# Kernel tuning notes

Measured on AMD Instinct MI355X. Metric: run time of the kernel, lower is better.

## Reference

```python
import jax, jax.numpy as jnp
import numpy as np

EPS = 1e-8
K_KNN = 20

def vn_lin(W, x):
    # W: [Cout, Cin], x: [B, Cin, 3, ...] -> [B, Cout, 3, ...]
    return jnp.einsum('oi,bi...->bo...', W, x)

def vn_relu(Wd, x):
    # VNLeakyReLU with negative_slope=0, share_nonlinearity=False
    d = jnp.einsum('oi,bi...->bo...', Wd, x)
    dot = jnp.sum(x * d, axis=2, keepdims=True)   # sum over 3-vector axis
    dsq = jnp.sum(d * d, axis=2, keepdims=True) + EPS
    return jnp.where(dot >= 0, x, x - (dot / dsq) * d)

def graph_feature_cross(p, k):
    # p: [B, N, 3] -> feat: [B, 3, 3, N, k]
    xx = jnp.sum(p * p, axis=-1)                       # [B,N]
    inner = jnp.einsum('bnd,bmd->bnm', p, p)           # [B,N,N]
    neg_dist = 2.0 * inner - xx[:, :, None] - xx[:, None, :]
    idx = jax.lax.top_k(neg_dist, k)[1]                # [B,N,k] nearest neighbors
    nbrs = jax.vmap(lambda pb, ib: pb[ib])(p, idx)     # [B,N,k,3]
    xr = jnp.broadcast_to(p[:, :, None, :], nbrs.shape)
    cross = jnp.cross(nbrs, xr)                        # [B,N,k,3]
    feat = jnp.stack([nbrs - xr, xr, cross], axis=3)   # [B,N,k,3(ch),3(vec)]
    return jnp.transpose(feat, (0, 3, 4, 1, 2))        # [B,3,3,N,k]

def setup_inputs() -> dict:
    key = jax.random.key(0)
    ks = jax.random.split(key, 9)
    B, N = 4, 2048
    H = 128           # hidden_dim // 3
    C_IN = 2 * H      # 256
    CC = 128          # c_dim // 3
    s_in = 1.0 / np.sqrt(C_IN)
    s_h = 1.0 / np.sqrt(H)
    return {
        'p': jax.random.normal(ks[0], (B, N, 3), dtype=jnp.float32),
        'fc_pos_W': jax.random.normal(ks[1], (C_IN, 3), dtype=jnp.float32) / np.sqrt(3.0),
        'blk_d0': jax.random.normal(ks[2], (5, C_IN, C_IN), dtype=jnp.float32) * s_in,
        'blk_W0': jax.random.normal(ks[3], (5, H, C_IN), dtype=jnp.float32) * s_in,
        'blk_d1': jax.random.normal(ks[4], (5, H, H), dtype=jnp.float32) * s_h,
        'blk_W1': jax.random.normal(ks[5], (5, H, H), dtype=jnp.float32) * s_h,
        'blk_Ws': jax.random.normal(ks[6], (5, H, C_IN), dtype=jnp.float32) * s_in,
        'fc_c_W': jax.random.normal(ks[7], (CC, H), dtype=jnp.float32) * s_h,
        'act_d': jax.random.normal(ks[8], (H, H), dtype=jnp.float32) * s_h,
    }

def reference(p, fc_pos_W, blk_d0, blk_W0, blk_d1, blk_W1, blk_Ws, fc_c_W, act_d):
    feat = graph_feature_cross(p, K_KNN)          # [B,3,3,N,k]
    x = vn_lin(fc_pos_W, feat)                    # [B,256,3,N,k]
    net = jnp.mean(x, axis=-1)                    # mean_pool over k -> [B,256,3,N]

    def block(i, x):
        h = vn_lin(blk_W0[i], vn_relu(blk_d0[i], x))
        dx = vn_lin(blk_W1[i], vn_relu(blk_d1[i], h))
        return vn_lin(blk_Ws[i], x) + dx          # shortcut (size_in != size_out)

    net = block(0, net)                           # [B,128,3,N]
    for i in range(1, 5):
        pooled = jnp.broadcast_to(jnp.mean(net, axis=3, keepdims=True), net.shape)
        net = block(i, jnp.concatenate([net, pooled], axis=1))
    net = jnp.mean(net, axis=3)                   # [B,128,3]
    c = vn_lin(fc_c_W, vn_relu(act_d, net))       # [B,128,3]
    return c.reshape(c.shape[0], -1)              # [B,384]
```

## Files before the change

kernel.cpp:

```cpp
#include <hip/hip_runtime.h>
#include <math.h>

#define N_PTS 2048
#define K_NN  20
#define K_D   10
#define WTOT  819200
#define NM_REP 8
#define NM_STRIDE 1536
#define NM_BLK (NM_REP*NM_STRIDE)
#define NBLK 256
#define BPB  64
#define ROWS 96
#define LDS_BYTES (2*ROWS*264*2)

typedef unsigned short u16;
typedef unsigned int   u32;
typedef _Float16 f16;
using half8   = __attribute__((ext_vector_type(8))) _Float16;
using floatx4 = __attribute__((ext_vector_type(4))) float;

__device__ __forceinline__ void split2h(float v, f16& h, f16& l) {
    h = (f16)v;
    l = (f16)((v - (float)h) * 1024.0f);
}

__device__ __forceinline__ float neg_dist(float4 q2, float4 c) {
    return fmaf(q2.x, c.x, fmaf(q2.y, c.y, fmaf(q2.z, c.z, -q2.w))) - c.w;
}

__global__ __launch_bounds__(256) void prep_kernel(
    const float* __restrict__ pts, float* __restrict__ m_out,
    const float* __restrict__ bd0, const float* __restrict__ bW0,
    const float* __restrict__ bd1, const float* __restrict__ bW1,
    const float* __restrict__ bWs, u16* __restrict__ Wswz,
    float* __restrict__ nm_acc)
{
    __shared__ float4 sp[N_PTS];
    if (blockIdx.x >= 1024) {
        int i = (blockIdx.x - 1024) * 256 + threadIdx.x;
        if (i >= WTOT) return;
        if (i < 5*NM_BLK + 32) nm_acc[i] = 0.f;
        float v; int base, K, local;
        if (i < 327680)      { int rel = i;          base = (rel/65536)*65536;            local = rel%65536; K = 256; v = bd0[rel]; }
        else if (i < 491520) { int rel = i - 327680; base = 327680 + (rel/32768)*32768;   local = rel%32768; K = 256; v = bW0[rel]; }
        else if (i < 573440) { int rel = i - 491520; base = 491520 + (rel/16384)*16384;   local = rel%16384; K = 128; v = bd1[rel]; }
        else if (i < 655360) { int rel = i - 573440; base = 573440 + (rel/16384)*16384;   local = rel%16384; K = 128; v = bW1[rel]; }
        else                 { int rel = i - 655360; base = 655360 + (rel/32768)*32768;   local = rel%32768; K = 256; v = bWs[rel]; }
        int m = local / K, k = local % K;
        int NKF = K >> 5;
        int mf = m >> 4, r = m & 15;
        int kf = k >> 5, q = (k >> 3) & 3, ii = k & 7;
        int lane = q*16 + r;
        int dst = base + ((mf*NKF + kf)*64 + lane)*8 + ii;
        f16 h, l; split2h(v, h, l);
        f16* W = (f16*)Wswz;
        W[dst] = h; W[WTOT + dst] = l;
        return;
    }

    const int b     = blockIdx.x >> 8;
    const int qbase = (blockIdx.x & 255) << 3;
    const int ql    = threadIdx.x >> 5;
    const int sl    = threadIdx.x & 31;
    const float* pb = pts + (size_t)b * N_PTS * 3;
    for (int i = threadIdx.x; i < N_PTS; i += 256) {
        float x = pb[i*3+0], y = pb[i*3+1], z = pb[i*3+2];
        sp[i] = make_float4(x, y, z, x*x + y*y + z*z);
    }
    __syncthreads();

    const int n = qbase + ql;
    const float4 q = sp[n];
    const float4 q2 = make_float4(2.f*q.x, 2.f*q.y, 2.f*q.z, q.w);

    float t[K_D];
#pragma unroll
    for (int s = 0; s < K_D; ++s) t[s] = -INFINITY;

    for (int j = 0; j < N_PTS/32; ++j) {
        float4 c = sp[j*32 + sl];
        float v = neg_dist(q2, c);
#pragma unroll
        for (int s = 0; s < K_D; ++s) {
            float nx = (s < K_D-1) ? t[s+1] : INFINITY;
            t[s] = fminf(fmaxf(t[s], v), nx);
        }
    }

    float head = t[K_D-1];
    float T = -INFINITY;
#pragma unroll 1
    for (int e = 0; e < K_NN; ++e) {
        float v = head; int w = sl;
#pragma unroll
        for (int off = 1; off < 32; off <<= 1) {
            float vo = __shfl_xor(v, off);
            int   wo = __shfl_xor(w, off);
            bool take = (vo > v) || (vo == v && wo < w);
            v = take ? vo : v;
            w = take ? wo : w;
        }
        T = v;
        if (w == sl) {
#pragma unroll
            for (int s = K_D-1; s > 0; --s) t[s] = t[s-1];
            t[0] = -INFINITY;
            head = t[K_D-1];
        }
    }

    float sx = 0.f, sy = 0.f, sz = 0.f;
    for (int j = 0; j < N_PTS/32; ++j) {
        float4 c = sp[j*32 + sl];
        float v = neg_dist(q2, c);
        if (v >= T) { sx += c.x; sy += c.y; sz += c.z; }
    }
#pragma unroll
    for (int off = 1; off < 32; off <<= 1) {
        sx += __shfl_xor(sx, off);
        sy += __shfl_xor(sy, off);
        sz += __shfl_xor(sz, off);
    }
    if (sl == 0) {
        const float inv = 1.0f / (float)K_NN;
        const int pt = b * N_PTS + n;
        m_out[pt*3+0] = sx * inv;
        m_out[pt*3+1] = sy * inv;
        m_out[pt*3+2] = sz * inv;
    }
}

template<int MF, int JF>
__device__ __forceinline__ void run_gemm_hi(
    const f16* __restrict__ Whi, size_t aoff,
    int NK, const f16* Blds, int bstride, int lane,
    floatx4 (&acc)[MF][JF])
{
    const int l15 = lane & 15;
    const int lq8 = (lane >> 4) * 8;
    half8 Aa[MF], Ab[MF];

    auto loada = [&](half8 (&dst)[MF], int kf) {
#pragma unroll
        for (int fm = 0; fm < MF; ++fm)
            dst[fm] = *(const half8*)(Whi + aoff + (size_t)(fm*NK + kf)*512 + (size_t)lane*8);
    };
    auto step = [&](half8 (&af)[MF], int kf) {
        half8 bq[JF];
#pragma unroll
        for (int fj = 0; fj < JF; ++fj)
            bq[fj] = *(const half8*)&Blds[(fj*16 + l15)*bstride + kf*32 + lq8];
#pragma unroll
        for (int fm = 0; fm < MF; ++fm)
#pragma unroll
            for (int fj = 0; fj < JF; ++fj)
                acc[fm][fj] = __builtin_amdgcn_mfma_f32_16x16x32_f16(af[fm], bq[fj], acc[fm][fj], 0, 0, 0);
    };

    loada(Aa, 0);
#pragma unroll 1
    for (int kf = 0; kf < NK; kf += 2) {
        loada(Ab, kf + 1);
        step(Aa, kf);
        if (kf + 2 < NK) loada(Aa, kf + 2);
        step(Ab, kf + 1);
    }
}

template<int MF, int JF>
__device__ __forceinline__ void run_gemm_split(
    const f16* __restrict__ Whi, const f16* __restrict__ Wlo, size_t aoff,
    int NK, const f16* Blds, int bstride, int lane,
    floatx4 (&acc)[MF][JF], floatx4 (&accL)[MF][JF])
{
    const int l15 = lane & 15;
    const int lq8 = (lane >> 4) * 8;
    half8 Aa[2*MF], Ab[2*MF];

    auto loada = [&](half8 (&dst)[2*MF], int kf) {
#pragma unroll
        for (int fm = 0; fm < MF; ++fm) {
            size_t fo = aoff + (size_t)(fm*NK + kf)*512 + (size_t)lane*8;
            dst[fm*2+0] = *(const half8*)(Whi + fo);
            dst[fm*2+1] = *(const half8*)(Wlo + fo);
        }
    };
    auto step = [&](half8 (&af)[2*MF], int kf) {
        half8 bq[JF];
#pragma unroll
        for (int fj = 0; fj < JF; ++fj)
            bq[fj] = *(const half8*)&Blds[(fj*16 + l15)*bstride + kf*32 + lq8];
#pragma unroll
        for (int fm = 0; fm < MF; ++fm)
#pragma unroll
            for (int fj = 0; fj < JF; ++fj) {
                acc[fm][fj]  = __builtin_amdgcn_mfma_f32_16x16x32_f16(af[fm*2+0], bq[fj], acc[fm][fj], 0, 0, 0);
                accL[fm][fj] = __builtin_amdgcn_mfma_f32_16x16x32_f16(af[fm*2+1], bq[fj], accL[fm][fj], 0, 0, 0);
            }
    };

    loada(Aa, 0);
#pragma unroll 1
    for (int kf = 0; kf < NK; kf += 2) {
        loada(Ab, kf + 1);
        step(Aa, kf);
        if (kf + 2 < NK) loada(Aa, kf + 2);
        step(Ab, kf + 1);
    }
}

__device__ __forceinline__ uint2 pack_res(floatx4 a, floatx4 aL) {
    u16 hh[4];
#pragma unroll
    for (int r = 0; r < 4; ++r) {
        f16 hv = (f16)(a[r] + aL[r] * (1.0f/1024.0f));
        hh[r] = *(u16*)&hv;
    }
    uint2 pv;
    pv.x = (u32)hh[0] | ((u32)hh[1] << 16);
    pv.y = (u32)hh[2] | ((u32)hh[3] << 16);
    return pv;
}

__device__ __forceinline__ uint2 pack_hi(floatx4 a) {
    u16 hh[4];
#pragma unroll
    for (int r = 0; r < 4; ++r) {
        f16 hv = (f16)a[r];
        hh[r] = *(u16*)&hv;
    }
    uint2 pv;
    pv.x = (u32)hh[0] | ((u32)hh[1] << 16);
    pv.y = (u32)hh[2] | ((u32)hh[3] << 16);
    return pv;
}

__global__ __launch_bounds__(512, 2) void resnet_kernel(
    const u16* __restrict__ Wswz,
    const float* __restrict__ pts, const float* __restrict__ m_buf,
    const float* __restrict__ fcW,
    float* __restrict__ nm_acc, int* __restrict__ cnt,
    const float* __restrict__ act_d, const float* __restrict__ fc_c,
    float* __restrict__ out)
{
    extern __shared__ char smem_raw[];
    f16*   X  = (f16*)smem_raw;
    f16*   Yd = X + ROWS*264;
    float* YC = (float*)Yd;

    const int tid   = threadIdx.x;
    const int bB    = blockIdx.x / BPB;
    const int lane  = tid & 63;
    const int wv    = tid >> 6;
    const int mwave = wv >> 1;
    const int ncol  = wv & 1;
    const f16* Whi = (const f16*)Wswz;
    const f16* Wlo = Whi + WTOT;

#pragma unroll 1
    for (int st = 0; st < 5; ++st) {
        const int offD0 = st*65536;
        const int offW0 = 327680 + st*32768;
        const int offD1 = 491520 + st*16384;
        const int offW1 = 573440 + st*16384;
        const int offWs = 655360 + st*32768;

        if (st == 0) {
            float* Hf = YC;
            const int ptbase = blockIdx.x * 32;
            for (int i = tid; i < 768; i += 512) Hf[i] = fcW[i];
            if (tid < 192) Hf[768 + tid] = (tid < 96) ? pts[ptbase*3 + tid]
                                                      : m_buf[ptbase*3 + tid - 96];
            __syncthreads();
#pragma unroll 1
            for (int it = 0; it < 6; ++it) {
                int idx = tid + 512*it;
                int r = idx >> 5;
                int cg = idx & 31;
                int l = r / 3, v = r - l*3;
                float pv0[3] = {Hf[768+l*3], Hf[768+l*3+1], Hf[768+l*3+2]};
                float mv0[3] = {Hf[864+l*3], Hf[864+l*3+1], Hf[864+l*3+2]};
                int v1 = (v==2) ? 0 : v+1;
                int v2 = (v==0) ? 2 : v-1;
                float av = mv0[v] - pv0[v];
                float bv = pv0[v];
                float cv = mv0[v1]*pv0[v2] - mv0[v2]*pv0[v1];
                half8 o;
#pragma unroll
                for (int k = 0; k < 8; ++k) {
                    int ch = cg*8 + k;
                    o[k] = (f16)(Hf[ch*3+0]*av + Hf[ch*3+1]*bv + Hf[ch*3+2]*cv);
                }
                *(half8*)&X[r*264 + cg*8] = o;
            }
            __syncthreads();
        }

        floatx4 acc4[2][3], accL4[2][3];
#pragma unroll
        for (int a = 0; a < 2; ++a)
#pragma unroll
            for (int b = 0; b < 3; ++b) { acc4[a][b] = (floatx4){0,0,0,0}; accL4[a][b] = (floatx4){0,0,0,0}; }

        {
            floatx4 acc[4][3];
#pragma unroll
            for (int a = 0; a < 4; ++a)
#pragma unroll
                for (int b = 0; b < 3; ++b) acc[a][b] = (floatx4){0,0,0,0};
            run_gemm_hi<4,3>(Whi, (size_t)offD0 + (size_t)mwave*16384, 8,
                             X + ncol*48*264, 264, lane, acc);
#pragma unroll
            for (int fm = 0; fm < 4; ++fm)
#pragma unroll
                for (int fj = 0; fj < 3; ++fj) {
                    int mloc = mwave*64 + fm*16 + (lane>>4)*4;
                    int jl   = ncol*48 + fj*16 + (lane & 15);
                    *(uint2*)&Yd[jl*264 + mloc] = pack_hi(acc[fm][fj]);
                }
        }
        __syncthreads();

        run_gemm_split<2,3>(Whi, Wlo, (size_t)offWs + (size_t)mwave*8192, 8,
                            X + ncol*48*264, 264, lane, acc4, accL4);

#pragma unroll 1
        for (int it = 0; it < 2; ++it) {
            int idx = tid + 512*it;
            int l = idx >> 5, cg = idx & 31;
            half8 xa = *(const half8*)&X[(l*3+0)*264 + cg*8];
            half8 xb = *(const half8*)&X[(l*3+1)*264 + cg*8];
            half8 xc = *(const half8*)&X[(l*3+2)*264 + cg*8];
            half8 da = *(const half8*)&Yd[(l*3+0)*264 + cg*8];
            half8 db = *(const half8*)&Yd[(l*3+1)*264 + cg*8];
            half8 dc = *(const half8*)&Yd[(l*3+2)*264 + cg*8];
            half8 ya, yb, yc;
#pragma unroll
            for (int k = 0; k < 8; ++k) {
                float x0 = (float)xa[k], x1 = (float)xb[k], x2 = (float)xc[k];
                float d0 = (float)da[k], d1 = (float)db[k], d2 = (float)dc[k];
                float dot = x0*d0 + x1*d1 + x2*d2;
                float y0, y1, y2;
                if (dot >= 0.f) { y0 = x0; y1 = x1; y2 = x2; }
                else {
                    float dsq = d0*d0 + d1*d1 + d2*d2 + 1e-8f;
                    float sc = dot / dsq;
                    y0 = x0 - sc*d0; y1 = x1 - sc*d1; y2 = x2 - sc*d2;
                }
                ya[k] = (f16)y0; yb[k] = (f16)y1; yc[k] = (f16)y2;
            }
            *(half8*)&Yd[(l*3+0)*264 + cg*8] = ya;
            *(half8*)&Yd[(l*3+1)*264 + cg*8] = yb;
            *(half8*)&Yd[(l*3+2)*264 + cg*8] = yc;
        }
        __syncthreads();

        {
            floatx4 acc[2][3], accL[2][3];
#pragma unroll
            for (int a = 0; a < 2; ++a)
#pragma unroll
                for (int b = 0; b < 3; ++b) { acc[a][b] = (floatx4){0,0,0,0}; accL[a][b] = (floatx4){0,0,0,0}; }
            run_gemm_split<2,3>(Whi, Wlo, (size_t)offW0 + (size_t)mwave*8192, 8,
                                Yd + ncol*48*264, 264, lane, acc, accL);
#pragma unroll
            for (int fm = 0; fm < 2; ++fm)
#pragma unroll
                for (int fj = 0; fj < 3; ++fj) {
                    int mloc = mwave*32 + fm*16 + (lane>>4)*4;
                    int jl   = ncol*48 + fj*16 + (lane & 15);
                    *(uint2*)&X[jl*136 + mloc] = pack_res(acc[fm][fj], accL[fm][fj]);
                }
        }
        __syncthreads();

        {
            floatx4 acc[2][3];
#pragma unroll
            for (int a = 0; a < 2; ++a)
#pragma unroll
                for (int b = 0; b < 3; ++b) acc[a][b] = (floatx4){0,0,0,0};
            run_gemm_hi<2,3>(Whi, (size_t)offD1 + (size_t)mwave*4096, 4,
                             X + ncol*48*136, 136, lane, acc);
#pragma unroll
            for (int fm = 0; fm < 2; ++fm)
#pragma unroll
                for (int fj = 0; fj < 3; ++fj) {
                    int mloc = mwave*32 + fm*16 + (lane>>4)*4;
                    int jl   = ncol*48 + fj*16 + (lane & 15);
                    *(uint2*)&Yd[jl*136 + mloc] = pack_hi(acc[fm][fj]);
                }
        }
        __syncthreads();

        {
            int l = tid >> 4, cg = tid & 15;
            half8 xa = *(const half8*)&X[(l*3+0)*136 + cg*8];
            half8 xb = *(const half8*)&X[(l*3+1)*136 + cg*8];
            half8 xc = *(const half8*)&X[(l*3+2)*136 + cg*8];
            half8 da = *(const half8*)&Yd[(l*3+0)*136 + cg*8];
            half8 db = *(const half8*)&Yd[(l*3+1)*136 + cg*8];
            half8 dc = *(const half8*)&Yd[(l*3+2)*136 + cg*8];
            half8 ya, yb, yc;
#pragma unroll
            for (int k = 0; k < 8; ++k) {
                float x0 = (float)xa[k], x1 = (float)xb[k], x2 = (float)xc[k];
                float d0 = (float)da[k], d1 = (float)db[k], d2 = (float)dc[k];
                float dot = x0*d0 + x1*d1 + x2*d2;
                float y0, y1, y2;
                if (dot >= 0.f) { y0 = x0; y1 = x1; y2 = x2; }
                else {
                    float dsq = d0*d0 + d1*d1 + d2*d2 + 1e-8f;
                    float sc = dot / dsq;
                    y0 = x0 - sc*d0; y1 = x1 - sc*d1; y2 = x2 - sc*d2;
                }
                ya[k] = (f16)y0; yb[k] = (f16)y1; yc[k] = (f16)y2;
            }
            *(half8*)&X[(l*3+0)*136 + cg*8] = ya;
            *(half8*)&X[(l*3+1)*136 + cg*8] = yb;
            *(half8*)&X[(l*3+2)*136 + cg*8] = yc;
        }
        __syncthreads();

        run_gemm_split<2,3>(Whi, Wlo, (size_t)offW1 + (size_t)mwave*4096, 4,
                            X + ncol*48*136, 136, lane, acc4, accL4);
        __syncthreads();

#pragma unroll
        for (int fm = 0; fm < 2; ++fm)
#pragma unroll
            for (int fj = 0; fj < 3; ++fj) {
                int mloc = mwave*32 + fm*16 + (lane>>4)*4;
                int jl   = ncol*48 + fj*16 + (lane & 15);
                floatx4 res;
#pragma unroll
                for (int r = 0; r < 4; ++r) res[r] = acc4[fm][fj][r] + accL4[fm][fj][r] * (1.0f/1024.0f);
                *(uint2*)&X[jl*264 + mloc] = pack_res(acc4[fm][fj], accL4[fm][fj]);
                *(floatx4*)&YC[jl*132 + mloc] = res;
            }
        __syncthreads();

        const int rsel = (blockIdx.x & (NM_REP-1)) * NM_STRIDE;
        float* nmS = nm_acc + (size_t)st*NM_BLK;
        if (tid < 384) {
            int v = tid >> 7, ch = tid & 127;
            float sum = 0.f;
#pragma unroll 1
            for (int pt = 0; pt < 32; ++pt) sum += YC[(pt*3+v)*132 + ch];
            atomicAdd(nmS + rsel + (bB*3+v)*128 + ch, sum);
        }
        asm volatile("s_waitcnt vmcnt(0)" ::: "memory");
        __syncthreads();
        if (tid == 0)
            __hip_atomic_fetch_add(&cnt[st*4+bB], 1, __ATOMIC_RELAXED, __HIP_MEMORY_SCOPE_AGENT);
        if (st == 4) break;

        if (tid == 0) {
            while (__hip_atomic_load(&cnt[st*4+bB], __ATOMIC_RELAXED, __HIP_MEMORY_SCOPE_AGENT) < BPB)
                __builtin_amdgcn_s_sleep(8);
        }
        __syncthreads();

        f16* nmT = Yd;
        if (tid < 384) {
            int v = tid >> 7, ch = tid & 127;
            float sum = 0.f;
#pragma unroll
            for (int rep = 0; rep < NM_REP; ++rep)
                sum += __hip_atomic_load(nmS + rep*NM_STRIDE + (bB*3+v)*128 + ch,
                                         __ATOMIC_RELAXED, __HIP_MEMORY_SCOPE_AGENT);
            nmT[tid] = (f16)(sum * (1.0f/2048.0f));
        }
        __syncthreads();
#pragma unroll 1
        for (int idx = tid; idx < 1536; idx += 512) {
            int r = idx >> 4;
            int cg = (idx & 15) + 16;
            int v = r % 3;
            *(half8*)&X[r*264 + cg*8] = *(const half8*)&nmT[v*128 + (cg-16)*8];
        }
        __syncthreads();
    }

    if (blockIdx.x < 4) {
        const int b = blockIdx.x;
        if (tid == 0) {
            while (__hip_atomic_load(&cnt[16+b], __ATOMIC_RELAXED, __HIP_MEMORY_SCOPE_AGENT) < BPB)
                __builtin_amdgcn_s_sleep(8);
        }
        __syncthreads();
        float* xs = (float*)smem_raw;
        float* ys = xs + 384;
        const float* nm4 = nm_acc + (size_t)4*NM_BLK;
        if (tid < 128) {
            int c = tid;
            float s0 = 0.f, s1 = 0.f, s2 = 0.f;
#pragma unroll
            for (int rep = 0; rep < NM_REP; ++rep) {
                s0 += __hip_atomic_load(nm4 + rep*NM_STRIDE + (b*3+0)*128 + c, __ATOMIC_RELAXED, __HIP_MEMORY_SCOPE_AGENT);
                s1 += __hip_atomic_load(nm4 + rep*NM_STRIDE + (b*3+1)*128 + c, __ATOMIC_RELAXED, __HIP_MEMORY_SCOPE_AGENT);
                s2 += __hip_atomic_load(nm4 + rep*NM_STRIDE + (b*3+2)*128 + c, __ATOMIC_RELAXED, __HIP_MEMORY_SCOPE_AGENT);
            }
            xs[c*3+0] = s0 * (1.0f/2048.0f);
            xs[c*3+1] = s1 * (1.0f/2048.0f);
            xs[c*3+2] = s2 * (1.0f/2048.0f);
        }
        __syncthreads();
        if (tid < 128) {
            int c = tid;
            float d0 = 0.f, d1 = 0.f, d2 = 0.f;
            for (int i = 0; i < 128; ++i) {
                float w = act_d[c*128 + i];
                d0 = fmaf(w, xs[i*3+0], d0);
                d1 = fmaf(w, xs[i*3+1], d1);
                d2 = fmaf(w, xs[i*3+2], d2);
            }
            float x0 = xs[c*3+0], x1 = xs[c*3+1], x2 = xs[c*3+2];
            float dot = x0*d0 + x1*d1 + x2*d2;
            float y0, y1, y2;
            if (dot >= 0.f) { y0 = x0; y1 = x1; y2 = x2; }
            else {
                float dsq = d0*d0 + d1*d1 + d2*d2 + 1e-8f;
                float sc = dot / dsq;
                y0 = x0 - sc*d0; y1 = x1 - sc*d1; y2 = x2 - sc*d2;
            }
            ys[c*3+0] = y0; ys[c*3+1] = y1; ys[c*3+2] = y2;
        }
        __syncthreads();
        if (tid < 128) {
            int c = tid;
            float o0 = 0.f, o1 = 0.f, o2 = 0.f;
            for (int i = 0; i < 128; ++i) {
                float w = fc_c[c*128 + i];
                o0 = fmaf(w, ys[i*3+0], o0);
                o1 = fmaf(w, ys[i*3+1], o1);
                o2 = fmaf(w, ys[i*3+2], o2);
            }
            out[b*384 + c*3 + 0] = o0;
            out[b*384 + c*3 + 1] = o1;
            out[b*384 + c*3 + 2] = o2;
        }
    }
}

extern "C" void kernel_launch(void* const* d_in, const int* in_sizes, int n_in,
                              void* d_out, int out_size, void* d_ws, size_t ws_size,
                              hipStream_t stream)
{
    const float* p      = (const float*)d_in[0];
    const float* fc_pos = (const float*)d_in[1];
    const float* bd0    = (const float*)d_in[2];
    const float* bW0    = (const float*)d_in[3];
    const float* bd1    = (const float*)d_in[4];
    const float* bW1    = (const float*)d_in[5];
    const float* bWs    = (const float*)d_in[6];
    const float* fc_c   = (const float*)d_in[7];
    const float* act_d  = (const float*)d_in[8];
    float* out = (float*)d_out;

    char* w = (char*)d_ws;
    float* m_buf  = (float*)w;  w += 98304;
    float* nm_acc = (float*)w;  w += (size_t)5*NM_BLK*4;
    int*   cnt    = (int*)w;    w += 128;
    u16*   Wswz   = (u16*)w;    w += (size_t)2*WTOT*2;

    static bool attr_set = false;
    if (!attr_set) {
        hipFuncSetAttribute((const void*)resnet_kernel,
                            hipFuncAttributeMaxDynamicSharedMemorySize, LDS_BYTES);
        attr_set = true;
    }

    prep_kernel<<<dim3(1024 + 3200), dim3(256), 0, stream>>>(
        p, m_buf, bd0, bW0, bd1, bW1, bWs, Wswz, nm_acc);

    resnet_kernel<<<dim3(NBLK), dim3(512), LDS_BYTES, stream>>>(
        Wswz, p, m_buf, fc_pos, nm_acc, cnt, act_d, fc_c, out);

    (void)in_sizes; (void)n_in; (void)out_size; (void)ws_size;
}
```

Before: 224.4 us.

## Overlap per-point half of block GEMMs with cross-block pooled-mean barrier wait

The first two GEMMs of each residual block (d0 and Ws) are split along K into the per-point-feature half and the pooled-mean half. The first half is computed before spinning on the cross-block counter for the previous stage's mean. The barrier wait, mean gather and broadcast into LDS now happen afterwards, followed by the remaining K half. This hides grid-wide synchronisation latency behind MFMA work, at the cost of keeping more accumulators live across the wait, which may raise register pressure.

```diff
diff --git a/kernel.cpp b/kernel.cpp
--- a/kernel.cpp
+++ b/kernel.cpp
@@ -133,7 +133,7 @@
 template<int MF, int JF>
 __device__ __forceinline__ void run_gemm_hi(
     const f16* __restrict__ Whi, size_t aoff,
-    int NK, const f16* Blds, int bstride, int lane,
+    int NK, int kf0, int kf1, const f16* Blds, int bstride, int lane,
     floatx4 (&acc)[MF][JF])
 {
     const int l15 = lane & 15;
@@ -157,12 +157,12 @@
                 acc[fm][fj] = __builtin_amdgcn_mfma_f32_16x16x32_f16(af[fm], bq[fj], acc[fm][fj], 0, 0, 0);
     };
 
-    loada(Aa, 0);
-#pragma unroll 1
-    for (int kf = 0; kf < NK; kf += 2) {
+    loada(Aa, kf0);
+#pragma unroll 1
+    for (int kf = kf0; kf < kf1; kf += 2) {
         loada(Ab, kf + 1);
         step(Aa, kf);
-        if (kf + 2 < NK) loada(Aa, kf + 2);
+        if (kf + 2 < kf1) loada(Aa, kf + 2);
         step(Ab, kf + 1);
     }
 }
@@ -170,7 +170,7 @@
 template<int MF, int JF>
 __device__ __forceinline__ void run_gemm_split(
     const f16* __restrict__ Whi, const f16* __restrict__ Wlo, size_t aoff,
-    int NK, const f16* Blds, int bstride, int lane,
+    int NK, int kf0, int kf1, const f16* Blds, int bstride, int lane,
     floatx4 (&acc)[MF][JF], floatx4 (&accL)[MF][JF])
 {
     const int l15 = lane & 15;
@@ -199,12 +199,12 @@
             }
     };
 
-    loada(Aa, 0);
-#pragma unroll 1
-    for (int kf = 0; kf < NK; kf += 2) {
+    loada(Aa, kf0);
+#pragma unroll 1
+    for (int kf = kf0; kf < kf1; kf += 2) {
         loada(Ab, kf + 1);
         step(Aa, kf);
-        if (kf + 2 < NK) loada(Aa, kf + 2);
+        if (kf + 2 < kf1) loada(Aa, kf + 2);
         step(Ab, kf + 1);
     }
 }
@@ -296,33 +296,78 @@
             __syncthreads();
         }
 
+        floatx4 acc1[4][3];
         floatx4 acc4[2][3], accL4[2][3];
 #pragma unroll
+        for (int a = 0; a < 4; ++a)
+#pragma unroll
+            for (int b = 0; b < 3; ++b) acc1[a][b] = (floatx4){0,0,0,0};
+#pragma unroll
         for (int a = 0; a < 2; ++a)
 #pragma unroll
             for (int b = 0; b < 3; ++b) { acc4[a][b] = (floatx4){0,0,0,0}; accL4[a][b] = (floatx4){0,0,0,0}; }
 
-        {
-            floatx4 acc[4][3];
-#pragma unroll
-            for (int a = 0; a < 4; ++a)
-#pragma unroll
-                for (int b = 0; b < 3; ++b) acc[a][b] = (floatx4){0,0,0,0};
-            run_gemm_hi<4,3>(Whi, (size_t)offD0 + (size_t)mwave*16384, 8,
-                             X + ncol*48*264, 264, lane, acc);
+        if (st == 0) {
+            run_gemm_hi<4,3>(Whi, (size_t)offD0 + (size_t)mwave*16384, 8, 0, 8,
+                             X + ncol*48*264, 264, lane, acc1);
 #pragma unroll
             for (int fm = 0; fm < 4; ++fm)
 #pragma unroll
                 for (int fj = 0; fj < 3; ++fj) {
                     int mloc = mwave*64 + fm*16 + (lane>>4)*4;
                     int jl   = ncol*48 + fj*16 + (lane & 15);
-                    *(uint2*)&Yd[jl*264 + mloc] = pack_hi(acc[fm][fj]);
-                }
-        }
-        __syncthreads();
-
-        run_gemm_split<2,3>(Whi, Wlo, (size_t)offWs + (size_t)mwave*8192, 8,
-                            X + ncol*48*264, 264, lane, acc4, accL4);
+                    *(uint2*)&Yd[jl*264 + mloc] = pack_hi(acc1[fm][fj]);
+                }
+            __syncthreads();
+            run_gemm_split<2,3>(Whi, Wlo, (size_t)offWs + (size_t)mwave*8192, 8, 0, 8,
+                                X + ncol*48*264, 264, lane, acc4, accL4);
+        } else {
+            run_gemm_hi<4,3>(Whi, (size_t)offD0 + (size_t)mwave*16384, 8, 0, 4,
+                             X + ncol*48*264, 264, lane, acc1);
+            run_gemm_split<2,3>(Whi, Wlo, (size_t)offWs + (size_t)mwave*8192, 8, 0, 4,
+                                X + ncol*48*264, 264, lane, acc4, accL4);
+
+            if (tid == 0) {
+                while (__hip_atomic_load(&cnt[(st-1)*4+bB], __ATOMIC_RELAXED, __HIP_MEMORY_SCOPE_AGENT) < BPB)
+                    __builtin_amdgcn_s_sleep(8);
+            }
+            __syncthreads();
+
+            float* nmSp = nm_acc + (size_t)(st-1)*NM_BLK;
+            f16* nmT = Yd;
+            if (tid < 384) {
+                int v = tid >> 7, ch = tid & 127;
+                float sum = 0.f;
+#pragma unroll
+                for (int rep = 0; rep < NM_REP; ++rep)
+                    sum += __hip_atomic_load(nmSp + rep*NM_STRIDE + (bB*3+v)*128 + ch,
+                                             __ATOMIC_RELAXED, __HIP_MEMORY_SCOPE_AGENT);
+                nmT[tid] = (f16)(sum * (1.0f/2048.0f));
+            }
+            __syncthreads();
+#pragma unroll 1
+            for (int idx = tid; idx < 1536; idx += 512) {
+                int r = idx >> 4;
+                int cg = (idx & 15) + 16;
+                int v = r % 3;
+                *(half8*)&X[r*264 + cg*8] = *(const half8*)&nmT[v*128 + (cg-16)*8];
+            }
+            __syncthreads();
+
+            run_gemm_hi<4,3>(Whi, (size_t)offD0 + (size_t)mwave*16384, 8, 4, 8,
+                             X + ncol*48*264, 264, lane, acc1);
+#pragma unroll
+            for (int fm = 0; fm < 4; ++fm)
+#pragma unroll
+                for (int fj = 0; fj < 3; ++fj) {
+                    int mloc = mwave*64 + fm*16 + (lane>>4)*4;
+                    int jl   = ncol*48 + fj*16 + (lane & 15);
+                    *(uint2*)&Yd[jl*264 + mloc] = pack_hi(acc1[fm][fj]);
+                }
+            __syncthreads();
+            run_gemm_split<2,3>(Whi, Wlo, (size_t)offWs + (size_t)mwave*8192, 8, 4, 8,
+                                X + ncol*48*264, 264, lane, acc4, accL4);
+        }
 
 #pragma unroll 1
         for (int it = 0; it < 2; ++it) {
@@ -361,7 +406,7 @@
             for (int a = 0; a < 2; ++a)
 #pragma unroll
                 for (int b = 0; b < 3; ++b) { acc[a][b] = (floatx4){0,0,0,0}; accL[a][b] = (floatx4){0,0,0,0}; }
-            run_gemm_split<2,3>(Whi, Wlo, (size_t)offW0 + (size_t)mwave*8192, 8,
+            run_gemm_split<2,3>(Whi, Wlo, (size_t)offW0 + (size_t)mwave*8192, 8, 0, 8,
                                 Yd + ncol*48*264, 264, lane, acc, accL);
 #pragma unroll
             for (int fm = 0; fm < 2; ++fm)
@@ -380,7 +425,7 @@
             for (int a = 0; a < 2; ++a)
 #pragma unroll
                 for (int b = 0; b < 3; ++b) acc[a][b] = (floatx4){0,0,0,0};
-            run_gemm_hi<2,3>(Whi, (size_t)offD1 + (size_t)mwave*4096, 4,
+            run_gemm_hi<2,3>(Whi, (size_t)offD1 + (size_t)mwave*4096, 4, 0, 4,
                              X + ncol*48*136, 136, lane, acc);
 #pragma unroll
             for (int fm = 0; fm < 2; ++fm)
@@ -422,7 +467,7 @@
         }
         __syncthreads();
 
-        run_gemm_split<2,3>(Whi, Wlo, (size_t)offW1 + (size_t)mwave*4096, 4,
+        run_gemm_split<2,3>(Whi, Wlo, (size_t)offW1 + (size_t)mwave*4096, 4, 0, 4,
                             X + ncol*48*136, 136, lane, acc4, accL4);
         __syncthreads();
 
@@ -453,33 +498,6 @@
         __syncthreads();
         if (tid == 0)
             __hip_atomic_fetch_add(&cnt[st*4+bB], 1, __ATOMIC_RELAXED, __HIP_MEMORY_SCOPE_AGENT);
-        if (st == 4) break;
-
-        if (tid == 0) {
-            while (__hip_atomic_load(&cnt[st*4+bB], __ATOMIC_RELAXED, __HIP_MEMORY_SCOPE_AGENT) < BPB)
-                __builtin_amdgcn_s_sleep(8);
-        }
-        __syncthreads();
-
-        f16* nmT = Yd;
-        if (tid < 384) {
-            int v = tid >> 7, ch = tid & 127;
-            float sum = 0.f;
-#pragma unroll
-            for (int rep = 0; rep < NM_REP; ++rep)
-                sum += __hip_atomic_load(nmS + rep*NM_STRIDE + (bB*3+v)*128 + ch,
-                                         __ATOMIC_RELAXED, __HIP_MEMORY_SCOPE_AGENT);
-            nmT[tid] = (f16)(sum * (1.0f/2048.0f));
-        }
-        __syncthreads();
-#pragma unroll 1
-        for (int idx = tid; idx < 1536; idx += 512) {
-            int r = idx >> 4;
-            int cg = (idx & 15) + 16;
-            int v = r % 3;
-            *(half8*)&X[r*264 + cg*8] = *(const half8*)&nmT[v*128 + (cg-16)*8];
-        }
-        __syncthreads();
     }
 
     if (blockIdx.x < 4) {
```

After: 215.4 us. -4.0%, faster.
